# Kernel optimization log

Measured on AMD Instinct MI355X. Metric: run time of the kernel, lower is better.

## Reference

```python
import jax, jax.numpy as jnp
import numpy as np

ANCHORS = np.array([[116.0, 90.0], [156.0, 198.0], [373.0, 326.0]], dtype=np.float32)
IMAGE_SIZE = 2048.0
IGNORE_THRES = 0.5
OBJ_SCALE = 100.0
NO_OBJ_SCALE = 1.0
EPS = 1e-16
BCE_EPS = 1e-12


def _wh_iou(anchors, gwh):
    # anchors: [A,2], gwh: [T,2] -> iou [A,T]
    aw, ah = anchors[:, 0:1], anchors[:, 1:2]            # [A,1]
    gw, gh = gwh[None, :, 0], gwh[None, :, 1]            # [1,T]
    inter = jnp.minimum(aw, gw) * jnp.minimum(ah, gh)
    union = aw * ah + gw * gh - inter
    return inter / (union + EPS)


def _bbox_iou_xywh(box1, box2):
    # boxes [T,4] in (cx, cy, w, h)
    b1x1, b1x2 = box1[:, 0] - box1[:, 2] / 2, box1[:, 0] + box1[:, 2] / 2
    b1y1, b1y2 = box1[:, 1] - box1[:, 3] / 2, box1[:, 1] + box1[:, 3] / 2
    b2x1, b2x2 = box2[:, 0] - box2[:, 2] / 2, box2[:, 0] + box2[:, 2] / 2
    b2y1, b2y2 = box2[:, 1] - box2[:, 3] / 2, box2[:, 1] + box2[:, 3] / 2
    iw = jnp.clip(jnp.minimum(b1x2, b2x2) - jnp.maximum(b1x1, b2x1), 0.0)
    ih = jnp.clip(jnp.minimum(b1y2, b2y2) - jnp.maximum(b1y1, b2y1), 0.0)
    inter = iw * ih
    a1 = (b1x2 - b1x1) * (b1y2 - b1y1)
    a2 = (b2x2 - b2x1) * (b2y2 - b2y1)
    return inter / (a1 + a2 - inter + EPS)


def _masked_mean(v, m):
    return jnp.sum(v * m) / jnp.maximum(jnp.sum(m), 1.0)


def setup_inputs() -> dict:
    key = jax.random.key(0)
    k1, k2, k3 = jax.random.split(key, 3)
    B, A, G, T = 32, 3, 256, 4096
    x = jax.random.normal(k1, (B, A * 5, G, G), jnp.float32) * 0.1
    tb = jax.random.randint(k2, (T, 1), 0, B).astype(jnp.float32)
    tcls = jnp.zeros((T, 1), jnp.float32)
    txywh = jax.random.uniform(k3, (T, 4), jnp.float32, 0.02, 0.98)
    targets = jnp.concatenate([tb, tcls, txywh], axis=1)
    return {"x": x, "targets": targets}


def reference(x, targets):
    B, G = x.shape[0], x.shape[2]
    A = ANCHORS.shape[0]
    stride = IMAGE_SIZE / G

    pred = x.reshape(B, A, 5, G, G).transpose(0, 1, 3, 4, 2)  # [B,A,G,G,5]
    cx = jax.nn.sigmoid(pred[..., 0])
    cy = jax.nn.sigmoid(pred[..., 1])
    w = pred[..., 2]
    h = pred[..., 3]
    pred_conf = jax.nn.sigmoid(pred[..., 4])

    grid_x = jnp.arange(G, dtype=jnp.float32).reshape(1, 1, 1, G)
    grid_y = jnp.arange(G, dtype=jnp.float32).reshape(1, 1, G, 1)
    anchors = jnp.asarray(ANCHORS) / stride                      # [A,2]
    aw = anchors[:, 0].reshape(1, A, 1, 1)
    ah = anchors[:, 1].reshape(1, A, 1, 1)

    pred_boxes = jnp.stack(
        [grid_x + cx, grid_y + cy, jnp.exp(w) * aw, jnp.exp(h) * ah], axis=-1
    )  # [B,A,G,G,4]
    output = jnp.concatenate(
        [pred_boxes.reshape(B, -1, 4) * stride, pred_conf.reshape(B, -1, 1)], axis=-1
    )

    # ---- build_targets (YOLOv3) ----
    tbox = targets[:, 2:6] * G                                   # [T,4] grid units
    gxy, gwh = tbox[:, :2], tbox[:, 2:]
    ious = _wh_iou(anchors, gwh)                                 # [A,T]
    best_n = jnp.argmax(ious, axis=0)                            # [T]
    b = targets[:, 0].astype(jnp.int32)
    gi = jnp.clip(jnp.floor(gxy[:, 0]), 0, G - 1).astype(jnp.int32)
    gj = jnp.clip(jnp.floor(gxy[:, 1]), 0, G - 1).astype(jnp.int32)

    zeros = jnp.zeros((B, A, G, G), jnp.float32)
    obj_mask = zeros.at[b, best_n, gj, gi].set(1.0)
    no_obj_mask = jnp.ones((B, A, G, G), jnp.float32).at[b, best_n, gj, gi].set(0.0)
    aidx = jnp.arange(A)
    keep = (ious.T <= IGNORE_THRES).astype(jnp.float32)          # [T,A]
    no_obj_mask = no_obj_mask.at[
        b[:, None], aidx[None, :], gj[:, None], gi[:, None]
    ].min(keep)

    tx = zeros.at[b, best_n, gj, gi].set(gxy[:, 0] - gi.astype(jnp.float32))
    ty = zeros.at[b, best_n, gj, gi].set(gxy[:, 1] - gj.astype(jnp.float32))
    tw = zeros.at[b, best_n, gj, gi].set(jnp.log(gwh[:, 0] / anchors[best_n, 0] + EPS))
    th = zeros.at[b, best_n, gj, gi].set(jnp.log(gwh[:, 1] / anchors[best_n, 1] + EPS))
    tconf = obj_mask

    pbt = pred_boxes[b, best_n, gj, gi]                          # [T,4]
    iou_scores = zeros.at[b, best_n, gj, gi].set(_bbox_iou_xywh(pbt, tbox))

    # ---- losses ----
    loss_x = _masked_mean((cx - tx) ** 2, obj_mask)
    loss_y = _masked_mean((cy - ty) ** 2, obj_mask)
    loss_w = _masked_mean((w - tw) ** 2, obj_mask)
    loss_h = _masked_mean((h - th) ** 2, obj_mask)
    loss_bbox = loss_x + loss_y + loss_w + loss_h
    bce = -(tconf * jnp.log(pred_conf + BCE_EPS)
            + (1.0 - tconf) * jnp.log(1.0 - pred_conf + BCE_EPS))
    loss_conf_obj = _masked_mean(bce, obj_mask)
    loss_conf_no_obj = _masked_mean(bce, no_obj_mask)
    loss_conf = OBJ_SCALE * loss_conf_obj + NO_OBJ_SCALE * loss_conf_no_obj
    loss_layer = loss_bbox + loss_conf

    # ---- metrics (side-effect scalars in torch; returned stop_gradient'd) ----
    conf50 = (pred_conf > 0.5).astype(jnp.float32)
    iou50 = (iou_scores > 0.5).astype(jnp.float32)
    iou75 = (iou_scores > 0.75).astype(jnp.float32)
    detected = conf50 * tconf
    conf_obj = _masked_mean(pred_conf, obj_mask)
    conf_no_obj = _masked_mean(pred_conf, no_obj_mask)
    precision = jnp.sum(iou50 * detected) / (jnp.sum(conf50) + EPS)
    recall50 = jnp.sum(iou50 * detected) / (jnp.sum(obj_mask) + EPS)
    recall75 = jnp.sum(iou75 * detected) / (jnp.sum(obj_mask) + EPS)
    metrics = jax.lax.stop_gradient(jnp.stack([
        loss_x, loss_y, loss_w, loss_h, loss_bbox, loss_conf, loss_layer,
        conf_obj, conf_no_obj, precision, recall50, recall75,
    ]))
    return output, loss_layer, metrics
```

## Files before the change

### kernel.cpp

```cpp
#include <hip/hip_runtime.h>
#include <cmath>

#define NA 3
#define HSIZE 8192
#define HMASK (HSIZE - 1)

typedef float v4f __attribute__((ext_vector_type(4)));


__device__ __forceinline__ float sigf(float v){ return 1.0f/(1.0f + expf(-v)); }
__device__ __forceinline__ unsigned hslot(unsigned key){
  return (key * 2654435761u) >> 19;
}

__global__ __launch_bounds__(256) void k_zero(int* __restrict__ p, int n){
  int i = blockIdx.x*256 + threadIdx.x;
  if (i < n) p[i] = 0;
}

__global__ __launch_bounds__(256) void k_targets(
    const float* __restrict__ targets, int T, int G, float stride,
    int* __restrict__ ocell, int* __restrict__ keyarr,
    int* __restrict__ A_key, int* __restrict__ A_val,
    int* __restrict__ B_key, int* __restrict__ B_bits, int* __restrict__ B_maxt)
{
  int t = blockIdx.x*256 + threadIdx.x;
  if (t >= T) return;
  const float* tr = targets + (size_t)t*6;
  int b = (int)tr[0];
  float gx = tr[2]*(float)G, gy = tr[3]*(float)G, gw = tr[4]*(float)G, gh = tr[5]*(float)G;
  float aw[NA] = {116.0f/stride, 156.0f/stride, 373.0f/stride};
  float ah[NA] = { 90.0f/stride, 198.0f/stride, 326.0f/stride};
  float best_iou = -1.0f; int best = 0; int bits = 0;
  #pragma unroll
  for (int a = 0; a < NA; ++a){
    float inter = fminf(aw[a], gw) * fminf(ah[a], gh);
    float uni   = aw[a]*ah[a] + gw*gh - inter;
    float iou   = inter / (uni + 1e-16f);
    if (iou > best_iou){ best_iou = iou; best = a; }
    if (iou > 0.5f) bits |= (1 << a);
  }
  bits |= (1 << best);
  int gi = (int)floorf(gx); gi = gi < 0 ? 0 : (gi > G-1 ? G-1 : gi);
  int gj = (int)floorf(gy); gj = gj < 0 ? 0 : (gj > G-1 ? G-1 : gj);
  int cell = (b*G + gj)*G + gi;
  int okey = cell*4 + best;
  ocell[t]  = okey;
  keyarr[t] = (cell << 3) | bits;

  unsigned s = hslot((unsigned)okey) & HMASK;
  for (;;){
    int prev = atomicCAS(&A_key[s], 0, okey+1);
    if (prev == 0 || prev == okey+1){ atomicMax(&A_val[s], t+1); break; }
    s = (s+1) & HMASK;
  }
  s = hslot((unsigned)cell) & HMASK;
  for (;;){
    int prev = atomicCAS(&B_key[s], 0, cell+1);
    if (prev == 0 || prev == cell+1){
      atomicOr(&B_bits[s], bits);
      atomicMax(&B_maxt[s], t+1);
      break;
    }
    s = (s+1) & HMASK;
  }
}

__global__ __launch_bounds__(256) void k_sparse(
    const float* __restrict__ x, const float* __restrict__ targets,
    int T, int G, float stride,
    const int* __restrict__ ocell, const int* __restrict__ keyarr,
    const int* __restrict__ A_key, const int* __restrict__ A_val,
    const int* __restrict__ B_key, const int* __restrict__ B_bits,
    const int* __restrict__ B_maxt, double* __restrict__ sums)
{
  int tid = threadIdx.x;
  int t = blockIdx.x*256 + tid;
  double v[12];
  #pragma unroll
  for (int k = 0; k < 12; ++k) v[k] = 0.0;

  if (t < T){
    const float* tr = targets + (size_t)t*6;
    int b = (int)tr[0];
    float gx = tr[2]*(float)G, gy = tr[3]*(float)G, gw = tr[4]*(float)G, gh = tr[5]*(float)G;
    float aw[NA] = {116.0f/stride, 156.0f/stride, 373.0f/stride};
    float ah[NA] = { 90.0f/stride, 198.0f/stride, 326.0f/stride};
    int okey = ocell[t];
    int myk  = keyarr[t];
    int cell = myk >> 3;
    int best = okey & 3;
    int gi = cell % G;
    int gj = (cell / G) % G;
    int GG = G*G;

    unsigned s = hslot((unsigned)okey) & HMASK;
    while (A_key[s] != okey+1) s = (s+1) & HMASK;
    bool owner = (A_val[s] == t+1);

    if (owner){
      float awb = aw[best], ahb = ah[best];
      const float* xp = x + ((size_t)(b*(NA*5) + best*5))*GG + (size_t)gj*G + gi;
      float x0 = xp[0], x1 = xp[(size_t)GG], x2 = xp[(size_t)2*GG],
            x3 = xp[(size_t)3*GG], x4 = xp[(size_t)4*GG];
      float cx = sigf(x0), cy = sigf(x1), w = x2, h = x3, conf = sigf(x4);
      float tx = gx - (float)gi, ty = gy - (float)gj;
      float tw = logf(gw/awb + 1e-16f), th = logf(gh/ahb + 1e-16f);
      v[3] = (double)((cx-tx)*(cx-tx));
      v[4] = (double)((cy-ty)*(cy-ty));
      v[5] = (double)((w-tw)*(w-tw));
      v[6] = (double)((h-th)*(h-th));
      v[7] = (double)(-logf(conf + 1e-12f));
      v[8] = (double)conf;
      float px = (float)gi + cx, py = (float)gj + cy;
      float pw = expf(w)*awb, ph = expf(h)*ahb;
      float iw = fminf(px + pw*0.5f, gx + gw*0.5f) - fmaxf(px - pw*0.5f, gx - gw*0.5f);
      float ih = fminf(py + ph*0.5f, gy + gh*0.5f) - fmaxf(py - ph*0.5f, gy - gh*0.5f);
      iw = fmaxf(iw, 0.0f); ih = fmaxf(ih, 0.0f);
      float inter = iw*ih;
      float iou = inter / (pw*ph + gw*gh - inter + 1e-16f);
      bool det = conf > 0.5f;
      v[9]  = (iou > 0.5f  && det) ? 1.0 : 0.0;
      v[10] = (iou > 0.75f && det) ? 1.0 : 0.0;
      v[11] = 1.0;
    }

    s = hslot((unsigned)cell) & HMASK;
    while (B_key[s] != cell+1) s = (s+1) & HMASK;
    if (B_maxt[s] == t+1){
      int bits = B_bits[s];
      #pragma unroll
      for (int a = 0; a < NA; ++a){
        if (bits & (1 << a)){
          float x4 = x[((size_t)(b*(NA*5) + a*5 + 4))*GG + (size_t)gj*G + gi];
          float conf = sigf(x4);
          v[0] += (double)(-logf(1.0f - conf + 1e-12f));
          v[1] += (double)conf;
          v[2] += 1.0;
        }
      }
    }
  }

  #pragma unroll
  for (int k = 0; k < 12; ++k){
    #pragma unroll
    for (int off = 32; off > 0; off >>= 1) v[k] += __shfl_down(v[k], off);
  }
  __shared__ double sred[4][12];
  int lane = tid & 63, wv = tid >> 6;
  if (lane == 0){
    #pragma unroll
    for (int k = 0; k < 12; ++k) sred[wv][k] = v[k];
  }
  __syncthreads();
  if (tid < 12){
    double sm = sred[0][tid] + sred[1][tid] + sred[2][tid] + sred[3][tid];
    unsafeAtomicAdd(&sums[3 + tid], sm);
  }
}

__global__ __launch_bounds__(256) void k_dense(
    const float* __restrict__ x, float* __restrict__ out,
    double* __restrict__ sums, int G, float stride, int total_cells)
{
  __shared__ float lds[256*41];
  int tid = threadIdx.x;
  int i = blockIdx.x*256 + tid;
  int cell = i*8;
  double nb = 0.0, cs = 0.0;
  int c50i = 0;

  if (cell < total_cells){
    int GG = G*G;
    int gx    = cell % G;
    int row   = cell / G;
    int gy    = row % G;
    int plane = row / G;
    int a     = plane % NA;
    float aw_all[NA] = {116.0f/stride, 156.0f/stride, 373.0f/stride};
    float ah_all[NA] = { 90.0f/stride, 198.0f/stride, 326.0f/stride};
    float aw = aw_all[a], ah = ah_all[a];

    size_t base = (size_t)plane*5*GG + (size_t)gy*G + gx;
    v4f v[5][2];
    #pragma unroll
    for (int c = 0; c < 5; ++c){
      const v4f* p = (const v4f*)(x + base + (size_t)c*GG);
      v[c][0] = p[0];
      v[c][1] = p[1];
    }

    float* myl = lds + tid*41;
    #pragma unroll
    for (int j = 0; j < 8; ++j){
      float p0 = v[0][j>>2][j&3];
      float p1 = v[1][j>>2][j&3];
      float p2 = v[2][j>>2][j&3];
      float p3 = v[3][j>>2][j&3];
      float p4 = v[4][j>>2][j&3];
      float cx   = 1.0f/(1.0f + expf(-p0));
      float cy   = 1.0f/(1.0f + expf(-p1));
      float pw   = expf(p2)*aw;
      float ph   = expf(p3)*ah;
      float conf = 1.0f/(1.0f + expf(-p4));
      myl[j*5+0] = ((float)(gx + j) + cx)*stride;
      myl[j*5+1] = ((float)gy + cy)*stride;
      myl[j*5+2] = pw*stride;
      myl[j*5+3] = ph*stride;
      myl[j*5+4] = conf;
      nb += (double)(-logf(1.0f - conf + 1e-12f));
      cs += (double)conf;
      c50i += (conf > 0.5f) ? 1 : 0;
    }
  }
  __syncthreads();

  int lane = tid & 63, wv = tid >> 6;
  {
    size_t waveBase = ((size_t)blockIdx.x*2048 + (size_t)wv*512)*5;
    if (waveBase < (size_t)total_cells*5){
      const float* wl = lds + (size_t)(wv*64)*41;
      #pragma unroll
      for (int c = 0; c < 10; ++c){
        int f = (c*64 + lane)*4;
        int owner = f / 40;
        int within = f - owner*40;
        const float* src = wl + owner*41 + within;
        v4f val;
        val.x = src[0]; val.y = src[1]; val.z = src[2]; val.w = src[3];
        __builtin_nontemporal_store(val, (v4f*)(out + waveBase + f));
      }
    }
  }

  double vals[3] = {nb, cs, (double)c50i};
  #pragma unroll
  for (int k = 0; k < 3; ++k){
    #pragma unroll
    for (int off = 32; off > 0; off >>= 1) vals[k] += __shfl_down(vals[k], off);
  }
  __shared__ double sred[4][3];
  if (lane == 0){
    sred[wv][0] = vals[0]; sred[wv][1] = vals[1]; sred[wv][2] = vals[2];
  }
  __syncthreads();
  if (tid < 3){
    double sm = sred[0][tid] + sred[1][tid] + sred[2][tid] + sred[3][tid];
    unsafeAtomicAdd(&sums[tid], sm);
  }
}

__global__ __launch_bounds__(64) void k_final(
    const double* __restrict__ sums, float* __restrict__ tail, double total_cells)
{
  if (threadIdx.x != 0) return;
  double nb_all = sums[0], conf_all = sums[1], c50_all = sums[2];
  double enb = sums[3], econf = sums[4], ecnt = sums[5];
  double lx = sums[6], ly = sums[7], lw = sums[8], lh = sums[9];
  double bce = sums[10], cobj = sums[11], i50 = sums[12], i75 = sums[13], nobj = sums[14];

  double dObj = fmax(nobj, 1.0);
  double n_noobj = total_cells - ecnt;
  double dNo  = fmax(n_noobj, 1.0);

  double loss_x = lx/dObj, loss_y = ly/dObj, loss_w = lw/dObj, loss_h = lh/dObj;
  double loss_bbox = loss_x + loss_y + loss_w + loss_h;
  double loss_conf_obj   = bce/dObj;
  double loss_conf_noobj = (nb_all - enb)/dNo;
  double loss_conf  = 100.0*loss_conf_obj + 1.0*loss_conf_noobj;
  double loss_layer = loss_bbox + loss_conf;
  double conf_obj   = cobj/dObj;
  double conf_noobj = (conf_all - econf)/dNo;
  double precision  = i50/(c50_all + 1e-16);
  double recall50   = i50/(nobj + 1e-16);
  double recall75   = i75/(nobj + 1e-16);

  tail[0]  = (float)loss_layer;
  tail[1]  = (float)loss_x;
  tail[2]  = (float)loss_y;
  tail[3]  = (float)loss_w;
  tail[4]  = (float)loss_h;
  tail[5]  = (float)loss_bbox;
  tail[6]  = (float)loss_conf;
  tail[7]  = (float)loss_layer;
  tail[8]  = (float)conf_obj;
  tail[9]  = (float)conf_noobj;
  tail[10] = (float)precision;
  tail[11] = (float)recall50;
  tail[12] = (float)recall75;
}

extern "C" void kernel_launch(void* const* d_in, const int* in_sizes, int n_in,
                              void* d_out, int out_size, void* d_ws, size_t ws_size,
                              hipStream_t stream) {
  const float* x       = (const float*)d_in[0];
  const float* targets = (const float*)d_in[1];
  float* out = (float*)d_out;

  const int B = 32;
  int GG = in_sizes[0] / (B * NA * 5);
  int G = (int)(sqrt((double)GG) + 0.5);
  int T = in_sizes[1] / 6;
  float stride = 2048.0f / (float)G;

  char* ws = (char*)d_ws;
  double* sums  = (double*)ws;
  int* A_key  = (int*)(ws + 128);
  int* A_val  = A_key + HSIZE;
  int* B_key  = A_val + HSIZE;
  int* B_bits = B_key + HSIZE;
  int* B_maxt = B_bits + HSIZE;
  int* ocell  = B_maxt + HSIZE;
  int* keyarr = ocell + T;

  int total_cells = B * NA * GG;
  int nzero = 32 + 5*HSIZE;
  int nblkZ = (nzero + 255) / 256;
  int nblkT = (T + 255) / 256;
  int nblkD = (total_cells/8 + 255) / 256;

  k_zero   <<<nblkZ, 256, 0, stream>>>((int*)ws, nzero);
  k_targets<<<nblkT, 256, 0, stream>>>(targets, T, G, stride, ocell, keyarr,
                                       A_key, A_val, B_key, B_bits, B_maxt);
  k_sparse <<<nblkT, 256, 0, stream>>>(x, targets, T, G, stride, ocell, keyarr,
                                       A_key, A_val, B_key, B_bits, B_maxt, sums);
  k_dense  <<<nblkD, 256, 0, stream>>>(x, out, sums, G, stride, total_cells);
  k_final  <<<1, 64, 0, stream>>>(sums, out + (size_t)total_cells*5, (double)total_cells);
}
```

Baseline: 258.3 us.

## Merge sparse and dense passes into one launch with fast math and smaller tiles

Folds the per-target sparse kernel into the dense kernel as extra leading blocks, which removes one launch and lets the sparse work overlap with the streaming dense pass. The dense part now handles 4 cells per thread instead of 8, which halves LDS use per block, and adds an occupancy hint to launch_bounds. It also switches the sigmoid, exp and log calls to fast intrinsics and does per-thread and per-wave accumulation in float instead of double. The fast intrinsics and float partial sums trade a little accuracy for fewer instructions.

```diff
diff --git a/kernel.cpp b/kernel.cpp
--- a/kernel.cpp
+++ b/kernel.cpp
@@ -9,6 +9,9 @@
 
 
 __device__ __forceinline__ float sigf(float v){ return 1.0f/(1.0f + expf(-v)); }
+__device__ __forceinline__ float fast_sig(float v){
+  return __builtin_amdgcn_rcpf(1.0f + __expf(-v));
+}
 __device__ __forceinline__ unsigned hslot(unsigned key){
   return (key * 2654435761u) >> 19;
 }
@@ -66,110 +69,108 @@
   }
 }
 
-__global__ __launch_bounds__(256) void k_sparse(
+__global__ __launch_bounds__(256, 7) void k_main(
     const float* __restrict__ x, const float* __restrict__ targets,
-    int T, int G, float stride,
+    float* __restrict__ out, double* __restrict__ sums,
+    int T, int G, float stride, int total_cells, int nblkT,
     const int* __restrict__ ocell, const int* __restrict__ keyarr,
     const int* __restrict__ A_key, const int* __restrict__ A_val,
     const int* __restrict__ B_key, const int* __restrict__ B_bits,
-    const int* __restrict__ B_maxt, double* __restrict__ sums)
+    const int* __restrict__ B_maxt)
 {
   int tid = threadIdx.x;
-  int t = blockIdx.x*256 + tid;
-  double v[12];
-  #pragma unroll
-  for (int k = 0; k < 12; ++k) v[k] = 0.0;
-
-  if (t < T){
-    const float* tr = targets + (size_t)t*6;
-    int b = (int)tr[0];
-    float gx = tr[2]*(float)G, gy = tr[3]*(float)G, gw = tr[4]*(float)G, gh = tr[5]*(float)G;
-    float aw[NA] = {116.0f/stride, 156.0f/stride, 373.0f/stride};
-    float ah[NA] = { 90.0f/stride, 198.0f/stride, 326.0f/stride};
-    int okey = ocell[t];
-    int myk  = keyarr[t];
-    int cell = myk >> 3;
-    int best = okey & 3;
-    int gi = cell % G;
-    int gj = (cell / G) % G;
-    int GG = G*G;
-
-    unsigned s = hslot((unsigned)okey) & HMASK;
-    while (A_key[s] != okey+1) s = (s+1) & HMASK;
-    bool owner = (A_val[s] == t+1);
-
-    if (owner){
-      float awb = aw[best], ahb = ah[best];
-      const float* xp = x + ((size_t)(b*(NA*5) + best*5))*GG + (size_t)gj*G + gi;
-      float x0 = xp[0], x1 = xp[(size_t)GG], x2 = xp[(size_t)2*GG],
-            x3 = xp[(size_t)3*GG], x4 = xp[(size_t)4*GG];
-      float cx = sigf(x0), cy = sigf(x1), w = x2, h = x3, conf = sigf(x4);
-      float tx = gx - (float)gi, ty = gy - (float)gj;
-      float tw = logf(gw/awb + 1e-16f), th = logf(gh/ahb + 1e-16f);
-      v[3] = (double)((cx-tx)*(cx-tx));
-      v[4] = (double)((cy-ty)*(cy-ty));
-      v[5] = (double)((w-tw)*(w-tw));
-      v[6] = (double)((h-th)*(h-th));
-      v[7] = (double)(-logf(conf + 1e-12f));
-      v[8] = (double)conf;
-      float px = (float)gi + cx, py = (float)gj + cy;
-      float pw = expf(w)*awb, ph = expf(h)*ahb;
-      float iw = fminf(px + pw*0.5f, gx + gw*0.5f) - fmaxf(px - pw*0.5f, gx - gw*0.5f);
-      float ih = fminf(py + ph*0.5f, gy + gh*0.5f) - fmaxf(py - ph*0.5f, gy - gh*0.5f);
-      iw = fmaxf(iw, 0.0f); ih = fmaxf(ih, 0.0f);
-      float inter = iw*ih;
-      float iou = inter / (pw*ph + gw*gh - inter + 1e-16f);
-      bool det = conf > 0.5f;
-      v[9]  = (iou > 0.5f  && det) ? 1.0 : 0.0;
-      v[10] = (iou > 0.75f && det) ? 1.0 : 0.0;
-      v[11] = 1.0;
-    }
-
-    s = hslot((unsigned)cell) & HMASK;
-    while (B_key[s] != cell+1) s = (s+1) & HMASK;
-    if (B_maxt[s] == t+1){
-      int bits = B_bits[s];
-      #pragma unroll
-      for (int a = 0; a < NA; ++a){
-        if (bits & (1 << a)){
-          float x4 = x[((size_t)(b*(NA*5) + a*5 + 4))*GG + (size_t)gj*G + gi];
-          float conf = sigf(x4);
-          v[0] += (double)(-logf(1.0f - conf + 1e-12f));
-          v[1] += (double)conf;
-          v[2] += 1.0;
+
+  if ((int)blockIdx.x < nblkT){
+    int t = blockIdx.x*256 + tid;
+    double v[12];
+    #pragma unroll
+    for (int k = 0; k < 12; ++k) v[k] = 0.0;
+
+    if (t < T){
+      const float* tr = targets + (size_t)t*6;
+      int b = (int)tr[0];
+      float gx = tr[2]*(float)G, gy = tr[3]*(float)G, gw = tr[4]*(float)G, gh = tr[5]*(float)G;
+      int okey = ocell[t];
+      int myk  = keyarr[t];
+      int cell = myk >> 3;
+      int best = okey & 3;
+      int gi = cell % G;
+      int gj = (cell / G) % G;
+      int GG = G*G;
+
+      unsigned s = hslot((unsigned)okey) & HMASK;
+      while (A_key[s] != okey+1) s = (s+1) & HMASK;
+      bool owner = (A_val[s] == t+1);
+
+      if (owner){
+        float awb = (best==0 ? 116.0f : (best==1 ? 156.0f : 373.0f)) / stride;
+        float ahb = (best==0 ?  90.0f : (best==1 ? 198.0f : 326.0f)) / stride;
+        const float* xp = x + ((size_t)(b*(NA*5) + best*5))*GG + (size_t)gj*G + gi;
+        float x0 = xp[0], x1 = xp[(size_t)GG], x2 = xp[(size_t)2*GG],
+              x3 = xp[(size_t)3*GG], x4 = xp[(size_t)4*GG];
+        float cx = sigf(x0), cy = sigf(x1), w = x2, h = x3, conf = sigf(x4);
+        float tx = gx - (float)gi, ty = gy - (float)gj;
+        float tw = logf(gw/awb + 1e-16f), th = logf(gh/ahb + 1e-16f);
+        v[3] = (double)((cx-tx)*(cx-tx));
+        v[4] = (double)((cy-ty)*(cy-ty));
+        v[5] = (double)((w-tw)*(w-tw));
+        v[6] = (double)((h-th)*(h-th));
+        v[7] = (double)(-logf(conf + 1e-12f));
+        v[8] = (double)conf;
+        float px = (float)gi + cx, py = (float)gj + cy;
+        float pw = expf(w)*awb, ph = expf(h)*ahb;
+        float iw = fminf(px + pw*0.5f, gx + gw*0.5f) - fmaxf(px - pw*0.5f, gx - gw*0.5f);
+        float ih = fminf(py + ph*0.5f, gy + gh*0.5f) - fmaxf(py - ph*0.5f, gy - gh*0.5f);
+        iw = fmaxf(iw, 0.0f); ih = fmaxf(ih, 0.0f);
+        float inter = iw*ih;
+        float iou = inter / (pw*ph + gw*gh - inter + 1e-16f);
+        bool det = conf > 0.5f;
+        v[9]  = (iou > 0.5f  && det) ? 1.0 : 0.0;
+        v[10] = (iou > 0.75f && det) ? 1.0 : 0.0;
+        v[11] = 1.0;
+      }
+
+      s = hslot((unsigned)cell) & HMASK;
+      while (B_key[s] != cell+1) s = (s+1) & HMASK;
+      if (B_maxt[s] == t+1){
+        int bits = B_bits[s];
+        #pragma unroll
+        for (int a = 0; a < NA; ++a){
+          if (bits & (1 << a)){
+            float x4 = x[((size_t)(b*(NA*5) + a*5 + 4))*GG + (size_t)gj*G + gi];
+            float conf = sigf(x4);
+            v[0] += (double)(-logf(1.0f - conf + 1e-12f));
+            v[1] += (double)conf;
+            v[2] += 1.0;
+          }
         }
       }
     }
-  }
-
-  #pragma unroll
-  for (int k = 0; k < 12; ++k){
-    #pragma unroll
-    for (int off = 32; off > 0; off >>= 1) v[k] += __shfl_down(v[k], off);
-  }
-  __shared__ double sred[4][12];
-  int lane = tid & 63, wv = tid >> 6;
-  if (lane == 0){
-    #pragma unroll
-    for (int k = 0; k < 12; ++k) sred[wv][k] = v[k];
-  }
-  __syncthreads();
-  if (tid < 12){
-    double sm = sred[0][tid] + sred[1][tid] + sred[2][tid] + sred[3][tid];
-    unsafeAtomicAdd(&sums[3 + tid], sm);
-  }
-}
-
-__global__ __launch_bounds__(256) void k_dense(
-    const float* __restrict__ x, float* __restrict__ out,
-    double* __restrict__ sums, int G, float stride, int total_cells)
-{
-  __shared__ float lds[256*41];
-  int tid = threadIdx.x;
-  int i = blockIdx.x*256 + tid;
-  int cell = i*8;
-  double nb = 0.0, cs = 0.0;
-  int c50i = 0;
+
+    #pragma unroll
+    for (int k = 0; k < 12; ++k){
+      #pragma unroll
+      for (int off = 32; off > 0; off >>= 1) v[k] += __shfl_down(v[k], off);
+    }
+    __shared__ double sred12[4][12];
+    int lane = tid & 63, wv = tid >> 6;
+    if (lane == 0){
+      #pragma unroll
+      for (int k = 0; k < 12; ++k) sred12[wv][k] = v[k];
+    }
+    __syncthreads();
+    if (tid < 12){
+      double sm = sred12[0][tid] + sred12[1][tid] + sred12[2][tid] + sred12[3][tid];
+      unsafeAtomicAdd(&sums[3 + tid], sm);
+    }
+    return;
+  }
+
+  __shared__ float lds[256*21];
+  int dblk = blockIdx.x - nblkT;
+  int i = dblk*256 + tid;
+  int cell = i*4;
+  float nb = 0.0f, cs = 0.0f; int c50 = 0;
 
   if (cell < total_cells){
     int GG = G*G;
@@ -178,55 +179,48 @@
     int gy    = row % G;
     int plane = row / G;
     int a     = plane % NA;
-    float aw_all[NA] = {116.0f/stride, 156.0f/stride, 373.0f/stride};
-    float ah_all[NA] = { 90.0f/stride, 198.0f/stride, 326.0f/stride};
-    float aw = aw_all[a], ah = ah_all[a];
+    float aw = (a==0 ? 116.0f : (a==1 ? 156.0f : 373.0f)) / stride;
+    float ah = (a==0 ?  90.0f : (a==1 ? 198.0f : 326.0f)) / stride;
 
     size_t base = (size_t)plane*5*GG + (size_t)gy*G + gx;
-    v4f v[5][2];
-    #pragma unroll
-    for (int c = 0; c < 5; ++c){
-      const v4f* p = (const v4f*)(x + base + (size_t)c*GG);
-      v[c][0] = p[0];
-      v[c][1] = p[1];
-    }
-
-    float* myl = lds + tid*41;
-    #pragma unroll
-    for (int j = 0; j < 8; ++j){
-      float p0 = v[0][j>>2][j&3];
-      float p1 = v[1][j>>2][j&3];
-      float p2 = v[2][j>>2][j&3];
-      float p3 = v[3][j>>2][j&3];
-      float p4 = v[4][j>>2][j&3];
-      float cx   = 1.0f/(1.0f + expf(-p0));
-      float cy   = 1.0f/(1.0f + expf(-p1));
-      float pw   = expf(p2)*aw;
-      float ph   = expf(p3)*ah;
-      float conf = 1.0f/(1.0f + expf(-p4));
+    v4f p0 = *(const v4f*)(x + base);
+    v4f p1 = *(const v4f*)(x + base + (size_t)GG);
+    v4f p2 = *(const v4f*)(x + base + (size_t)2*GG);
+    v4f p3 = *(const v4f*)(x + base + (size_t)3*GG);
+    v4f p4 = *(const v4f*)(x + base + (size_t)4*GG);
+
+    float* myl = lds + tid*21;
+    #pragma unroll
+    for (int j = 0; j < 4; ++j){
+      float cx   = fast_sig(p0[j]);
+      float cy   = fast_sig(p1[j]);
+      float pw   = __expf(p2[j])*aw;
+      float ph   = __expf(p3[j])*ah;
+      float conf = fast_sig(p4[j]);
       myl[j*5+0] = ((float)(gx + j) + cx)*stride;
       myl[j*5+1] = ((float)gy + cy)*stride;
       myl[j*5+2] = pw*stride;
       myl[j*5+3] = ph*stride;
       myl[j*5+4] = conf;
-      nb += (double)(-logf(1.0f - conf + 1e-12f));
-      cs += (double)conf;
-      c50i += (conf > 0.5f) ? 1 : 0;
+      nb -= __logf(1.0f - conf + 1e-12f);
+      cs += conf;
+      c50 += (conf > 0.5f) ? 1 : 0;
     }
   }
   __syncthreads();
 
   int lane = tid & 63, wv = tid >> 6;
   {
-    size_t waveBase = ((size_t)blockIdx.x*2048 + (size_t)wv*512)*5;
-    if (waveBase < (size_t)total_cells*5){
-      const float* wl = lds + (size_t)(wv*64)*41;
-      #pragma unroll
-      for (int c = 0; c < 10; ++c){
-        int f = (c*64 + lane)*4;
-        int owner = f / 40;
-        int within = f - owner*40;
-        const float* src = wl + owner*41 + within;
+    size_t waveBase = ((size_t)dblk*1024 + (size_t)(wv*256))*5;
+    size_t totalF = (size_t)total_cells*5;
+    const float* wl = lds + (size_t)(wv*64)*21;
+    #pragma unroll
+    for (int c = 0; c < 5; ++c){
+      int f = (c*64 + lane)*4;
+      if (waveBase + (size_t)f < totalF){
+        int owner = f / 20;
+        int within = f - owner*20;
+        const float* src = wl + owner*21 + within;
         v4f val;
         val.x = src[0]; val.y = src[1]; val.z = src[2]; val.w = src[3];
         __builtin_nontemporal_store(val, (v4f*)(out + waveBase + f));
@@ -234,19 +228,21 @@
     }
   }
 
-  double vals[3] = {nb, cs, (double)c50i};
+  float vals[3] = {nb, cs, (float)c50};
   #pragma unroll
   for (int k = 0; k < 3; ++k){
     #pragma unroll
     for (int off = 32; off > 0; off >>= 1) vals[k] += __shfl_down(vals[k], off);
   }
-  __shared__ double sred[4][3];
+  __shared__ double sred3[4][3];
   if (lane == 0){
-    sred[wv][0] = vals[0]; sred[wv][1] = vals[1]; sred[wv][2] = vals[2];
+    sred3[wv][0] = (double)vals[0];
+    sred3[wv][1] = (double)vals[1];
+    sred3[wv][2] = (double)vals[2];
   }
   __syncthreads();
   if (tid < 3){
-    double sm = sred[0][tid] + sred[1][tid] + sred[2][tid] + sred[3][tid];
+    double sm = sred3[0][tid] + sred3[1][tid] + sred3[2][tid] + sred3[3][tid];
     unsafeAtomicAdd(&sums[tid], sm);
   }
 }
@@ -318,13 +314,14 @@
   int nzero = 32 + 5*HSIZE;
   int nblkZ = (nzero + 255) / 256;
   int nblkT = (T + 255) / 256;
-  int nblkD = (total_cells/8 + 255) / 256;
+  int nblkD = (total_cells + 1023) / 1024;
 
   k_zero   <<<nblkZ, 256, 0, stream>>>((int*)ws, nzero);
   k_targets<<<nblkT, 256, 0, stream>>>(targets, T, G, stride, ocell, keyarr,
                                        A_key, A_val, B_key, B_bits, B_maxt);
-  k_sparse <<<nblkT, 256, 0, stream>>>(x, targets, T, G, stride, ocell, keyarr,
-                                       A_key, A_val, B_key, B_bits, B_maxt, sums);
-  k_dense  <<<nblkD, 256, 0, stream>>>(x, out, sums, G, stride, total_cells);
+  k_main   <<<nblkT + nblkD, 256, 0, stream>>>(x, targets, out, sums,
+                                       T, G, stride, total_cells, nblkT,
+                                       ocell, keyarr,
+                                       A_key, A_val, B_key, B_bits, B_maxt);
   k_final  <<<1, 64, 0, stream>>>(sums, out + (size_t)total_cells*5, (double)total_cells);
 }
```

After: 259.4 us. About the same (+0.5%).
